# Kernel tuning notes

Measured on AMD Instinct MI355X. Metric: run time of the kernel, lower is better.

## Reference

```python
import jax, jax.numpy as jnp
import numpy as np

BN_EPS = 1e-5

def _bn(h, gamma, beta, mean, var):
    # inference-mode BatchNorm1d
    return (h - mean) * jax.lax.rsqrt(var + BN_EPS) * gamma + beta


def setup_inputs() -> dict:
    key = jax.random.key(0)
    ks = jax.random.split(key, 16)
    N, E, D_in, D, L = 100000, 640000, 256, 128, 3
    s = 0.05
    return {
        "x": jax.random.normal(ks[0], (N, D_in), jnp.float32),
        "edge_index": jax.random.randint(ks[1], (2, E), 0, N, jnp.int32),
        "W_in": jax.random.normal(ks[2], (D_in, D), jnp.float32) * s,
        "b_in": jax.random.normal(ks[3], (D,), jnp.float32) * s,
        "bn_in_gamma": jax.random.uniform(ks[4], (D,), jnp.float32, 0.5, 1.5),
        "bn_in_beta": jax.random.normal(ks[5], (D,), jnp.float32) * s,
        "bn_in_mean": jax.random.normal(ks[6], (D,), jnp.float32) * s,
        "bn_in_var": jax.random.uniform(ks[7], (D,), jnp.float32, 0.5, 1.5),
        "Wl": jax.random.normal(ks[8], (L, D, D), jnp.float32) * s,
        "bl": jax.random.normal(ks[9], (L, D), jnp.float32) * s,
        "Wr": jax.random.normal(ks[10], (L, D, D), jnp.float32) * s,
        "bn_gamma": jax.random.uniform(ks[11], (L, D), jnp.float32, 0.5, 1.5),
        "bn_beta": jax.random.normal(ks[12], (L, D), jnp.float32) * s,
        "bn_mean": jax.random.normal(ks[13], (L, D), jnp.float32) * s,
        "bn_var": jax.random.uniform(ks[14], (L, D), jnp.float32, 0.5, 1.5),
    }


def reference(x, edge_index, W_in, b_in, bn_in_gamma, bn_in_beta, bn_in_mean,
              bn_in_var, Wl, bl, Wr, bn_gamma, bn_beta, bn_mean, bn_var):
    N = x.shape[0]
    src, dst = edge_index[0], edge_index[1]
    # in-degree (clamped to 1 so isolated nodes aggregate to 0, matching PyG mean)
    deg = jax.ops.segment_sum(jnp.ones_like(dst, jnp.float32), dst, num_segments=N)
    deg = jnp.maximum(deg, 1.0)[:, None]  # [N, 1]

    # input projection + BN + ReLU (dropout = identity in eval)
    h = jax.nn.relu(_bn(x @ W_in + b_in, bn_in_gamma, bn_in_beta, bn_in_mean, bn_in_var))

    L = Wl.shape[0]
    for l in range(L):
        # SAGEConv(mean): lin_l(mean_j h_j) + lin_r(h_i)
        agg = jax.ops.segment_sum(h[src], dst, num_segments=N) / deg  # [N, D]
        h_new = agg @ Wl[l] + bl[l] + h @ Wr[l]
        h_new = jax.nn.relu(_bn(h_new, bn_gamma[l], bn_beta[l], bn_mean[l], bn_var[l]))
        h = h + h_new  # residual
    return h
```

## Files before the change

### kernel.cpp

```cpp
#include <hip/hip_runtime.h>

#define BN_EPS 1e-5f

typedef __bf16 bf16x8 __attribute__((ext_vector_type(8)));
typedef float f32x4 __attribute__((ext_vector_type(4)));
typedef unsigned int uint;
typedef unsigned short ushort;

__device__ __forceinline__ ushort f2bf(float f) {
  union { float f; uint u; } v; v.f = f;
  uint r = v.u + 0x7FFF + ((v.u >> 16) & 1);
  return (ushort)(r >> 16);
}
__device__ __forceinline__ float bf2f_lo(uint u) {
  union { uint i; float f; } v; v.i = u << 16; return v.f;
}
__device__ __forceinline__ float bf2f_hi(uint u) {
  union { uint i; float f; } v; v.i = u & 0xffff0000u; return v.f;
}
__device__ __forceinline__ uint pack2(float a, float b) {
  return (uint)f2bf(a) | ((uint)f2bf(b) << 16);
}


__global__ void prep_weights_fm(const float* __restrict__ W_in, const float* __restrict__ Wl,
                                const float* __restrict__ Wr, ushort* __restrict__ Bfm) {
  int p = blockIdx.x * 256 + threadIdx.x;
  int mat = p >> 12;
  int rem = p & 4095;
  int half = rem >> 11;
  int rem2 = rem & 2047;
  int nt = rem2 >> 8, kt2 = (rem2 >> 6) & 3, lane = rem2 & 63;
  int n = nt * 16 + (lane & 15);
  int k0 = (half * 4 + kt2) * 32 + (lane >> 4) * 8;
  ushort tmp[8];
  #pragma unroll
  for (int j = 0; j < 8; ++j) {
    int k = k0 + j;
    float v;
    if (mat == 0) v = W_in[k * 128 + n];
    else {
      int l = mat - 1;
      v = (k < 128) ? Wl[l * 16384 + k * 128 + n] : Wr[l * 16384 + (k - 128) * 128 + n];
    }
    tmp[j] = f2bf(v);
  }
  *(uint4*)&Bfm[(size_t)p * 8] = *(const uint4*)tmp;
}


__global__ void reserve_kernel(const int* __restrict__ cnt, int* __restrict__ rowbeg,
                               int* __restrict__ cursor, int N) {
  int tid = threadIdx.x;
  int i = blockIdx.x * 256 + tid;
  int v = (i < N) ? cnt[i] : 0;
  int lane = tid & 63;
  int x = v;
  #pragma unroll
  for (int off = 1; off < 64; off <<= 1) {
    int y = __shfl_up(x, off, 64);
    if (lane >= off) x += y;
  }
  int ret = 0;
  if (lane == 63) ret = atomicAdd(cursor, x);
  int base = __shfl(ret, 63);
  if (i < N) rowbeg[i] = base + x - v;
}

__global__ void fill_kernel(const int* __restrict__ src, const int* __restrict__ dst,
                            const int* __restrict__ rowbeg, int* __restrict__ cur,
                            int* __restrict__ col, int E) {
  int e = blockIdx.x * 256 + threadIdx.x;
  if (e < E) {
    int d = dst[e];
    int p = rowbeg[d] + atomicAdd(&cur[d], 1);
    col[p] = src[e];
  }
}


__global__ void agg_kernel(const int* __restrict__ rowbeg, const int* __restrict__ deg,
                           const int* __restrict__ col,
                           const ushort* __restrict__ h, ushort* __restrict__ agg, int N) {
  int node = blockIdx.x * 16 + (threadIdx.x >> 4);
  if (node >= N) return;
  int lane = threadIdx.x & 15;
  const ushort* hp = h + lane * 8;
  int beg = rowbeg[node];
  int d = deg[node];
  float di = 1.0f / (float)(d > 0 ? d : 1);
  int end = beg + d;
  float a0 = 0.f, a1 = 0.f, a2 = 0.f, a3 = 0.f;
  float a4 = 0.f, a5 = 0.f, a6 = 0.f, a7 = 0.f;
  #pragma unroll 1
  for (int e = beg; e < end; e += 8) {
    int cc[8];
    #pragma unroll
    for (int j = 0; j < 8; ++j) {
      int idx = e + j;
      cc[j] = col[idx < end ? idx : e];
    }
    uint4 v[8];
    #pragma unroll
    for (int j = 0; j < 8; ++j)
      v[j] = *(const uint4*)(hp + (size_t)cc[j] * 128);
    #pragma unroll
    for (int j = 1; j < 8; ++j)
      if (e + j >= end) { v[j].x = 0u; v[j].y = 0u; v[j].z = 0u; v[j].w = 0u; }
    #pragma unroll
    for (int j = 0; j < 8; ++j) {
      a0 += bf2f_lo(v[j].x); a1 += bf2f_hi(v[j].x);
      a2 += bf2f_lo(v[j].y); a3 += bf2f_hi(v[j].y);
      a4 += bf2f_lo(v[j].z); a5 += bf2f_hi(v[j].z);
      a6 += bf2f_lo(v[j].w); a7 += bf2f_hi(v[j].w);
    }
  }
  uint4 o;
  o.x = pack2(a0 * di, a1 * di);
  o.y = pack2(a2 * di, a3 * di);
  o.z = pack2(a4 * di, a5 * di);
  o.w = pack2(a6 * di, a7 * di);
  *(uint4*)(agg + (size_t)node * 128 + lane * 8) = o;
}


template<bool F32OUT>
__global__ __launch_bounds__(256, 4)
void gemm_layer(const ushort* __restrict__ A0, const ushort* __restrict__ A1,
                const ushort* __restrict__ Bfm, const float* __restrict__ bias,
                const float* __restrict__ gamma, const float* __restrict__ beta,
                const float* __restrict__ mean, const float* __restrict__ var,
                const ushort* __restrict__ residual, void* __restrict__ out, int N) {
  __shared__ float Cb_all[4 * 16 * 68];
  int tid = threadIdx.x, wave = tid >> 6, lane = tid & 63;
  int wm = wave >> 1, wn = wave & 1, quad = lane >> 4, l16 = lane & 15;
  int m0 = blockIdx.x * 64;

  int rowm[2];
  #pragma unroll
  for (int mt = 0; mt < 2; ++mt) {
    int r = m0 + wm * 32 + mt * 16 + l16;
    rowm[mt] = r < N ? r : N - 1;
  }

  uint4 a_buf[2][2], b_buf[2][4];
  #pragma unroll
  for (int mt = 0; mt < 2; ++mt)
    a_buf[0][mt] = *(const uint4*)(A0 + (size_t)rowm[mt] * 128 + quad * 8);
  {
    const ushort* bp = Bfm + (size_t)(wn * 4 * 256 + lane) * 8;
    #pragma unroll
    for (int nt = 0; nt < 4; ++nt)
      b_buf[0][nt] = *(const uint4*)(bp + nt * 2048);
  }

  f32x4 acc[2][4] = {};

  #pragma unroll
  for (int kt = 0; kt < 8; ++kt) {
    if (kt < 7) {
      int k1 = kt + 1;
      const ushort* bse = (k1 < 4) ? A0 : A1;
      int ko = (k1 & 3) * 32 + quad * 8;
      #pragma unroll
      for (int mt = 0; mt < 2; ++mt)
        a_buf[k1 & 1][mt] = *(const uint4*)(bse + (size_t)rowm[mt] * 128 + ko);
      const ushort* bp = Bfm + ((size_t)(k1 >> 2) * 16384 +
                                (size_t)((wn * 4) * 256 + (k1 & 3) * 64 + lane) * 8);
      #pragma unroll
      for (int nt = 0; nt < 4; ++nt)
        b_buf[k1 & 1][nt] = *(const uint4*)(bp + nt * 2048);
    }
    __builtin_amdgcn_sched_barrier(0);
    #pragma unroll
    for (int mt = 0; mt < 2; ++mt) {
      bf16x8 af = __builtin_bit_cast(bf16x8, a_buf[kt & 1][mt]);
      #pragma unroll
      for (int nt = 0; nt < 4; ++nt)
        acc[mt][nt] = __builtin_amdgcn_mfma_f32_16x16x32_bf16(
            af, __builtin_bit_cast(bf16x8, b_buf[kt & 1][nt]), acc[mt][nt], 0, 0, 0);
    }
  }

  #pragma unroll
  for (int nt = 0; nt < 4; ++nt) {
    int c = wn * 64 + nt * 16 + l16;
    float sc = gamma[c] * rsqrtf(var[c] + BN_EPS);
    float sh = beta[c] - mean[c] * sc;
    float bi = bias[c];
    #pragma unroll
    for (int mt = 0; mt < 2; ++mt)
      #pragma unroll
      for (int r = 0; r < 4; ++r)
        acc[mt][nt][r] = fmaxf((acc[mt][nt][r] + bi) * sc + sh, 0.f);
  }

  float* Cb = Cb_all + wave * (16 * 68);
  #pragma unroll
  for (int mt = 0; mt < 2; ++mt) {
    #pragma unroll
    for (int nt = 0; nt < 4; ++nt)
      #pragma unroll
      for (int r = 0; r < 4; ++r)
        Cb[(quad * 4 + r) * 68 + nt * 16 + l16] = acc[mt][nt][r];
    #pragma unroll
    for (int i = 0; i < 4; ++i) {
      int idx = i * 64 + lane, rowl = idx >> 4, seg = idx & 15;
      int grow = m0 + wm * 32 + mt * 16 + rowl;
      if (grow < N) {
        float4 vv = *(float4*)&Cb[rowl * 68 + seg * 4];
        uint2 rv = *(const uint2*)(residual + (size_t)grow * 128 + wn * 64 + seg * 4);
        vv.x += bf2f_lo(rv.x); vv.y += bf2f_hi(rv.x);
        vv.z += bf2f_lo(rv.y); vv.w += bf2f_hi(rv.y);
        if (F32OUT) {
          *(float4*)((float*)out + (size_t)grow * 128 + wn * 64 + seg * 4) = vv;
        } else {
          uint2 o;
          o.x = pack2(vv.x, vv.y); o.y = pack2(vv.z, vv.w);
          *(uint2*)((ushort*)out + (size_t)grow * 128 + wn * 64 + seg * 4) = o;
        }
      }
    }
  }
}


__global__ __launch_bounds__(256, 4)
void gemm_in_hist(const float* __restrict__ X, const ushort* __restrict__ Bfm,
                  const float* __restrict__ bias,
                  const float* __restrict__ gamma, const float* __restrict__ beta,
                  const float* __restrict__ mean, const float* __restrict__ var,
                  ushort* __restrict__ out,
                  const int* __restrict__ dst, int* __restrict__ cnt,
                  int N, int E, int GB) {
  __shared__ float Cb_all[4 * 16 * 68];
  if (blockIdx.x >= GB) {
    int e = (blockIdx.x - GB) * 256 + threadIdx.x;
    if (e < E) atomicAdd(&cnt[dst[e]], 1);
    return;
  }
  int tid = threadIdx.x, wave = tid >> 6, lane = tid & 63;
  int wm = wave >> 1, wn = wave & 1, quad = lane >> 4, l16 = lane & 15;
  int m0 = blockIdx.x * 64;

  int rowm[2];
  #pragma unroll
  for (int mt = 0; mt < 2; ++mt) {
    int r = m0 + wm * 32 + mt * 16 + l16;
    rowm[mt] = r < N ? r : N - 1;
  }

  float4 f_buf[2][2][2];
  uint4 b_buf[2][4];
  #pragma unroll
  for (int mt = 0; mt < 2; ++mt) {
    const float* p = X + (size_t)rowm[mt] * 256 + quad * 8;
    f_buf[0][mt][0] = *(const float4*)p;
    f_buf[0][mt][1] = *(const float4*)(p + 4);
  }
  {
    const ushort* bp = Bfm + (size_t)(wn * 4 * 256 + lane) * 8;
    #pragma unroll
    for (int nt = 0; nt < 4; ++nt)
      b_buf[0][nt] = *(const uint4*)(bp + nt * 2048);
  }

  f32x4 acc[2][4] = {};

  #pragma unroll
  for (int kt = 0; kt < 8; ++kt) {
    if (kt < 7) {
      int k1 = kt + 1;
      int ko = k1 * 32 + quad * 8;
      #pragma unroll
      for (int mt = 0; mt < 2; ++mt) {
        const float* p = X + (size_t)rowm[mt] * 256 + ko;
        f_buf[k1 & 1][mt][0] = *(const float4*)p;
        f_buf[k1 & 1][mt][1] = *(const float4*)(p + 4);
      }
      const ushort* bp = Bfm + ((size_t)(k1 >> 2) * 16384 +
                                (size_t)((wn * 4) * 256 + (k1 & 3) * 64 + lane) * 8);
      #pragma unroll
      for (int nt = 0; nt < 4; ++nt)
        b_buf[k1 & 1][nt] = *(const uint4*)(bp + nt * 2048);
    }
    __builtin_amdgcn_sched_barrier(0);
    #pragma unroll
    for (int mt = 0; mt < 2; ++mt) {
      float4 lo = f_buf[kt & 1][mt][0], hi = f_buf[kt & 1][mt][1];
      uint4 av;
      av.x = pack2(lo.x, lo.y); av.y = pack2(lo.z, lo.w);
      av.z = pack2(hi.x, hi.y); av.w = pack2(hi.z, hi.w);
      bf16x8 af = __builtin_bit_cast(bf16x8, av);
      #pragma unroll
      for (int nt = 0; nt < 4; ++nt)
        acc[mt][nt] = __builtin_amdgcn_mfma_f32_16x16x32_bf16(
            af, __builtin_bit_cast(bf16x8, b_buf[kt & 1][nt]), acc[mt][nt], 0, 0, 0);
    }
  }

  #pragma unroll
  for (int nt = 0; nt < 4; ++nt) {
    int c = wn * 64 + nt * 16 + l16;
    float sc = gamma[c] * rsqrtf(var[c] + BN_EPS);
    float sh = beta[c] - mean[c] * sc;
    float bi = bias[c];
    #pragma unroll
    for (int mt = 0; mt < 2; ++mt)
      #pragma unroll
      for (int r = 0; r < 4; ++r)
        acc[mt][nt][r] = fmaxf((acc[mt][nt][r] + bi) * sc + sh, 0.f);
  }

  float* Cb = Cb_all + wave * (16 * 68);
  #pragma unroll
  for (int mt = 0; mt < 2; ++mt) {
    #pragma unroll
    for (int nt = 0; nt < 4; ++nt)
      #pragma unroll
      for (int r = 0; r < 4; ++r)
        Cb[(quad * 4 + r) * 68 + nt * 16 + l16] = acc[mt][nt][r];
    #pragma unroll
    for (int i = 0; i < 4; ++i) {
      int idx = i * 64 + lane, rowl = idx >> 4, seg = idx & 15;
      int grow = m0 + wm * 32 + mt * 16 + rowl;
      if (grow < N) {
        float4 vv = *(float4*)&Cb[rowl * 68 + seg * 4];
        uint2 o;
        o.x = pack2(vv.x, vv.y); o.y = pack2(vv.z, vv.w);
        *(uint2*)(out + (size_t)grow * 128 + wn * 64 + seg * 4) = o;
      }
    }
  }
}


extern "C" void kernel_launch(void* const* d_in, const int* in_sizes, int n_in,
                              void* d_out, int out_size, void* d_ws, size_t ws_size,
                              hipStream_t stream) {
  const float* x      = (const float*)d_in[0];
  const int*   eidx   = (const int*)d_in[1];
  const float* W_in   = (const float*)d_in[2];
  const float* b_in   = (const float*)d_in[3];
  const float* bng_in = (const float*)d_in[4];
  const float* bnb_in = (const float*)d_in[5];
  const float* bnm_in = (const float*)d_in[6];
  const float* bnv_in = (const float*)d_in[7];
  const float* Wl     = (const float*)d_in[8];
  const float* bl     = (const float*)d_in[9];
  const float* Wr     = (const float*)d_in[10];
  const float* bng    = (const float*)d_in[11];
  const float* bnb    = (const float*)d_in[12];
  const float* bnm    = (const float*)d_in[13];
  const float* bnv    = (const float*)d_in[14];

  const int N = in_sizes[0] / 256;
  const int E = in_sizes[1] / 2;
  const int NB = (N + 255) / 256;
  const int* src = eidx;
  const int* dst = eidx + E;

  char* ws = (char*)d_ws;
  size_t off = 0;
  auto alloc = [&](size_t bytes) {
    void* p = ws + off;
    off = (off + bytes + 255) & ~(size_t)255;
    return p;
  };
  int* zreg     = (int*)alloc((size_t)(2 * N + 1) * 4);
  int* cnt      = zreg;
  int* cur      = zreg + N;
  int* cursor   = zreg + 2 * N;
  int* rowbeg   = (int*)alloc((size_t)N * 4);
  int* col      = (int*)alloc((size_t)E * 4);
  ushort* Bfm   = (ushort*)alloc(4 * 32768 * 2);
  ushort* hA    = (ushort*)alloc((size_t)N * 128 * 2);
  ushort* hB    = (ushort*)alloc((size_t)N * 128 * 2);
  ushort* agg   = (ushort*)alloc((size_t)N * 128 * 2);
  (void)ws_size; (void)n_in; (void)out_size;

  const int EB = (E + 255) / 256;
  const int GB = (N + 63) / 64;

  hipMemsetAsync(zreg, 0, (size_t)(2 * N + 1) * 4, stream);
  prep_weights_fm<<<64, 256, 0, stream>>>(W_in, Wl, Wr, Bfm);

  gemm_in_hist<<<GB + EB, 256, 0, stream>>>(x, Bfm, b_in, bng_in, bnb_in, bnm_in, bnv_in,
                                            hA, dst, cnt, N, E, GB);

  reserve_kernel<<<NB, 256, 0, stream>>>(cnt, rowbeg, cursor, N);
  fill_kernel<<<EB, 256, 0, stream>>>(src, dst, rowbeg, cur, col, E);

  ushort* hbuf[2] = { hA, hB };
  for (int l = 0; l < 3; ++l) {
    const ushort* h_in = hbuf[l & 1];
    agg_kernel<<<(N + 15) / 16, 256, 0, stream>>>(rowbeg, cnt, col, h_in, agg, N);
    const ushort* BfmL = Bfm + (size_t)(l + 1) * 32768;
    const float* biasL = bl + l * 128;
    if (l < 2) {
      gemm_layer<false><<<GB, 256, 0, stream>>>(agg, h_in, BfmL, biasL,
          bng + l * 128, bnb + l * 128, bnm + l * 128, bnv + l * 128,
          h_in, (void*)hbuf[(l + 1) & 1], N);
    } else {
      gemm_layer<true><<<GB, 256, 0, stream>>>(agg, h_in, BfmL, biasL,
          bng + l * 128, bnb + l * 128, bnm + l * 128, bnv + l * 128,
          h_in, d_out, N);
    }
  }
}
```

Measured before the change: 432.8 us.

## Gather neighbor features from an FP8 E4M3 copy to halve aggregation traffic

Each GEMM epilogue now also writes an 8-bit E4M3-style copy of the node features. The aggregation kernel gathers from this copy, reading 8 bytes per lane instead of 16, to cut random-access gather bandwidth. Buffers are reshuffled so the aggregation output and the next layer's h share storage, which needs a __syncthreads and dropped restrict qualifiers because the GEMM writes in place over its A0 input. The cost is lower precision in the mean aggregation, a risk to accuracy tolerance, plus an extra store in each epilogue.

```diff
diff --git a/kernel.cpp b/kernel.cpp
--- a/kernel.cpp
+++ b/kernel.cpp
@@ -6,6 +6,7 @@
 typedef float f32x4 __attribute__((ext_vector_type(4)));
 typedef unsigned int uint;
 typedef unsigned short ushort;
+typedef unsigned char uchar;
 
 __device__ __forceinline__ ushort f2bf(float f) {
   union { float f; uint u; } v; v.f = f;
@@ -20,6 +21,17 @@
 }
 __device__ __forceinline__ uint pack2(float a, float b) {
   return (uint)f2bf(a) | ((uint)f2bf(b) << 16);
+}
+
+__device__ __forceinline__ uint f2e4m3(float f) {
+  union { float f; uint u; } v; v.f = f * 0x1p-120f;
+  uint r = v.u + 0x7FFFF + ((v.u >> 20) & 1);
+  uint u8 = r >> 20;
+  return u8 > 0x7Eu ? 0x7Eu : u8;
+}
+__device__ __forceinline__ float e4m32f(uint u8) {
+  union { uint u; float f; } v; v.u = (u8 & 0x7Fu) << 20;
+  return v.f * 0x1p120f;
 }
 
 
@@ -81,11 +93,11 @@
 
 __global__ void agg_kernel(const int* __restrict__ rowbeg, const int* __restrict__ deg,
                            const int* __restrict__ col,
-                           const ushort* __restrict__ h, ushort* __restrict__ agg, int N) {
+                           const uchar* __restrict__ h8, ushort* __restrict__ agg, int N) {
   int node = blockIdx.x * 16 + (threadIdx.x >> 4);
   if (node >= N) return;
   int lane = threadIdx.x & 15;
-  const ushort* hp = h + lane * 8;
+  const uchar* hp = h8 + lane * 8;
   int beg = rowbeg[node];
   int d = deg[node];
   float di = 1.0f / (float)(d > 0 ? d : 1);
@@ -100,19 +112,19 @@
       int idx = e + j;
       cc[j] = col[idx < end ? idx : e];
     }
-    uint4 v[8];
+    uint2 v[8];
     #pragma unroll
     for (int j = 0; j < 8; ++j)
-      v[j] = *(const uint4*)(hp + (size_t)cc[j] * 128);
+      v[j] = *(const uint2*)(hp + (size_t)cc[j] * 128);
     #pragma unroll
     for (int j = 1; j < 8; ++j)
-      if (e + j >= end) { v[j].x = 0u; v[j].y = 0u; v[j].z = 0u; v[j].w = 0u; }
+      if (e + j >= end) { v[j].x = 0u; v[j].y = 0u; }
     #pragma unroll
     for (int j = 0; j < 8; ++j) {
-      a0 += bf2f_lo(v[j].x); a1 += bf2f_hi(v[j].x);
-      a2 += bf2f_lo(v[j].y); a3 += bf2f_hi(v[j].y);
-      a4 += bf2f_lo(v[j].z); a5 += bf2f_hi(v[j].z);
-      a6 += bf2f_lo(v[j].w); a7 += bf2f_hi(v[j].w);
+      a0 += e4m32f(v[j].x);        a1 += e4m32f(v[j].x >> 8);
+      a2 += e4m32f(v[j].x >> 16);  a3 += e4m32f(v[j].x >> 24);
+      a4 += e4m32f(v[j].y);        a5 += e4m32f(v[j].y >> 8);
+      a6 += e4m32f(v[j].y >> 16);  a7 += e4m32f(v[j].y >> 24);
     }
   }
   uint4 o;
@@ -126,11 +138,12 @@
 
 template<bool F32OUT>
 __global__ __launch_bounds__(256, 4)
-void gemm_layer(const ushort* __restrict__ A0, const ushort* __restrict__ A1,
+void gemm_layer(const ushort* A0, const ushort* __restrict__ A1,
                 const ushort* __restrict__ Bfm, const float* __restrict__ bias,
                 const float* __restrict__ gamma, const float* __restrict__ beta,
                 const float* __restrict__ mean, const float* __restrict__ var,
-                const ushort* __restrict__ residual, void* __restrict__ out, int N) {
+                const ushort* residual, void* out,
+                uchar* __restrict__ out8, int N) {
   __shared__ float Cb_all[4 * 16 * 68];
   int tid = threadIdx.x, wave = tid >> 6, lane = tid & 63;
   int wm = wave >> 1, wn = wave & 1, quad = lane >> 4, l16 = lane & 15;
@@ -194,6 +207,8 @@
       for (int r = 0; r < 4; ++r)
         acc[mt][nt][r] = fmaxf((acc[mt][nt][r] + bi) * sc + sh, 0.f);
   }
+
+  __syncthreads();
 
   float* Cb = Cb_all + wave * (16 * 68);
   #pragma unroll
@@ -218,6 +233,9 @@
           uint2 o;
           o.x = pack2(vv.x, vv.y); o.y = pack2(vv.z, vv.w);
           *(uint2*)((ushort*)out + (size_t)grow * 128 + wn * 64 + seg * 4) = o;
+          uint u8 = f2e4m3(vv.x) | (f2e4m3(vv.y) << 8) |
+                    (f2e4m3(vv.z) << 16) | (f2e4m3(vv.w) << 24);
+          *(uint*)(out8 + (size_t)grow * 128 + wn * 64 + seg * 4) = u8;
         }
       }
     }
@@ -230,7 +248,7 @@
                   const float* __restrict__ bias,
                   const float* __restrict__ gamma, const float* __restrict__ beta,
                   const float* __restrict__ mean, const float* __restrict__ var,
-                  ushort* __restrict__ out,
+                  ushort* __restrict__ out, uchar* __restrict__ out8,
                   const int* __restrict__ dst, int* __restrict__ cnt,
                   int N, int E, int GB) {
   __shared__ float Cb_all[4 * 16 * 68];
@@ -329,6 +347,9 @@
         uint2 o;
         o.x = pack2(vv.x, vv.y); o.y = pack2(vv.z, vv.w);
         *(uint2*)(out + (size_t)grow * 128 + wn * 64 + seg * 4) = o;
+        uint u8 = f2e4m3(vv.x) | (f2e4m3(vv.y) << 8) |
+                  (f2e4m3(vv.z) << 16) | (f2e4m3(vv.w) << 24);
+        *(uint*)(out8 + (size_t)grow * 128 + wn * 64 + seg * 4) = u8;
       }
     }
   }
@@ -374,9 +395,9 @@
   int* rowbeg   = (int*)alloc((size_t)N * 4);
   int* col      = (int*)alloc((size_t)E * 4);
   ushort* Bfm   = (ushort*)alloc(4 * 32768 * 2);
-  ushort* hA    = (ushort*)alloc((size_t)N * 128 * 2);
-  ushort* hB    = (ushort*)alloc((size_t)N * 128 * 2);
-  ushort* agg   = (ushort*)alloc((size_t)N * 128 * 2);
+  ushort* bufA  = (ushort*)alloc((size_t)N * 128 * 2);
+  ushort* bufB  = (ushort*)alloc((size_t)N * 128 * 2);
+  uchar* h8     = (uchar*)alloc((size_t)N * 128);
   (void)ws_size; (void)n_in; (void)out_size;
 
   const int EB = (E + 255) / 256;
@@ -386,25 +407,25 @@
   prep_weights_fm<<<64, 256, 0, stream>>>(W_in, Wl, Wr, Bfm);
 
   gemm_in_hist<<<GB + EB, 256, 0, stream>>>(x, Bfm, b_in, bng_in, bnb_in, bnm_in, bnv_in,
-                                            hA, dst, cnt, N, E, GB);
+                                            bufA, h8, dst, cnt, N, E, GB);
 
   reserve_kernel<<<NB, 256, 0, stream>>>(cnt, rowbeg, cursor, N);
   fill_kernel<<<EB, 256, 0, stream>>>(src, dst, rowbeg, cur, col, E);
 
-  ushort* hbuf[2] = { hA, hB };
   for (int l = 0; l < 3; ++l) {
-    const ushort* h_in = hbuf[l & 1];
-    agg_kernel<<<(N + 15) / 16, 256, 0, stream>>>(rowbeg, cnt, col, h_in, agg, N);
+    ushort* h_in   = (l & 1) ? bufB : bufA;
+    ushort* aggbuf = (l & 1) ? bufA : bufB;
+    agg_kernel<<<(N + 15) / 16, 256, 0, stream>>>(rowbeg, cnt, col, h8, aggbuf, N);
     const ushort* BfmL = Bfm + (size_t)(l + 1) * 32768;
     const float* biasL = bl + l * 128;
     if (l < 2) {
-      gemm_layer<false><<<GB, 256, 0, stream>>>(agg, h_in, BfmL, biasL,
+      gemm_layer<false><<<GB, 256, 0, stream>>>(aggbuf, h_in, BfmL, biasL,
           bng + l * 128, bnb + l * 128, bnm + l * 128, bnv + l * 128,
-          h_in, (void*)hbuf[(l + 1) & 1], N);
+          h_in, (void*)aggbuf, h8, N);
     } else {
-      gemm_layer<true><<<GB, 256, 0, stream>>>(agg, h_in, BfmL, biasL,
+      gemm_layer<true><<<GB, 256, 0, stream>>>(aggbuf, h_in, BfmL, biasL,
           bng + l * 128, bnb + l * 128, bnm + l * 128, bnv + l * 128,
-          h_in, d_out, N);
-    }
-  }
-}
+          h_in, d_out, nullptr, N);
+    }
+  }
+}
```

Result: no change. 425.8 us (-1.6%).
